# Kernel tuning notes

Hardware: AMD Instinct MI355X
Metric: run time of the kernel (lower is better)

## Reference

```python
import jax, jax.numpy as jnp
import numpy as np

N = 50000   # nodes
E = 600000  # edges
F = 128     # num_node_features
H = 128     # hidden_channels
C = 10      # num_classes
G = 64      # graphs in batch


def setup_inputs() -> dict:
    key = jax.random.key(0)
    ks = jax.random.split(key, 12)
    x = jax.random.normal(ks[0], (N, F), jnp.float32)
    edge_index = jax.random.randint(ks[1], (2, E), 0, N, dtype=jnp.int32)
    batch = jnp.sort(jax.random.randint(ks[2], (N,), 0, G, dtype=jnp.int32))
    def glorot(k, shape):
        lim = np.sqrt(6.0 / (shape[0] + shape[1])).astype(np.float32)
        return jax.random.uniform(k, shape, jnp.float32, -lim, lim)
    return {
        "x": x,
        "edge_index": edge_index,
        "batch": batch,
        "W1": glorot(ks[3], (F, H)), "b1": jnp.zeros((H,), jnp.float32),
        "W2": glorot(ks[4], (H, H)), "b2": jnp.zeros((H,), jnp.float32),
        "W3": glorot(ks[5], (H, H)), "b3": jnp.zeros((H,), jnp.float32),
        "Wl": glorot(ks[6], (H, C)), "bl": jnp.zeros((C,), jnp.float32),
    }


def reference(x, edge_index, batch, W1, b1, W2, b2, W3, b3, Wl, bl):
    # GCNConv: add self-loops, symmetric degree normalization D^-1/2 A D^-1/2
    src0, dst0 = edge_index[0], edge_index[1]
    loop = jnp.arange(N, dtype=src0.dtype)
    src = jnp.concatenate([src0, loop])
    dst = jnp.concatenate([dst0, loop])
    deg = jax.ops.segment_sum(jnp.ones_like(dst, jnp.float32), dst, num_segments=N)
    dinv = jnp.where(deg > 0, jax.lax.rsqrt(deg), 0.0)
    norm = dinv[src] * dinv[dst]  # [E+N]

    def conv(h, W, b):
        h = h @ W                                  # [N, H] transform first (PyG GCNConv)
        msg = h[src] * norm[:, None]               # gather + normalize
        return jax.ops.segment_sum(msg, dst, num_segments=N) + b  # scatter-add

    h = jax.nn.relu(conv(x, W1, b1))
    h = jax.nn.relu(conv(h, W2, b2))
    h = conv(h, W3, b3)

    # global_mean_pool over batch ids
    counts = jax.ops.segment_sum(jnp.ones((N,), jnp.float32), batch, num_segments=G)
    pooled = jax.ops.segment_sum(h, batch, num_segments=G) / jnp.maximum(counts, 1.0)[:, None]
    return pooled @ Wl + bl  # [G, C]
```

## Files before the change

### kernel.cpp

```cpp
#include <hip/hip_runtime.h>
#include <hip/hip_bf16.h>

#define NN 50000
#define EE 600000
#define FF 128
#define HH 128
#define CC 10
#define GG 64
#define SB 256
#define NBSCAN ((NN + SB - 1) / SB)

typedef unsigned int uint32;
typedef unsigned short ushort16;
typedef __attribute__((ext_vector_type(8))) short short8;
typedef __attribute__((ext_vector_type(4))) float f32x4;

__device__ __forceinline__ ushort16 f2bf(float f) {
    __hip_bfloat16 b = __float2bfloat16(f);
    return *reinterpret_cast<ushort16*>(&b);
}
__device__ __forceinline__ uint32 pack2bf(float a, float b) {
    return (uint32)f2bf(a) | ((uint32)f2bf(b) << 16);
}
__device__ __forceinline__ int q8(float f) {
    return __float2int_rn(fminf(fmaxf(f * 16.f, -127.f), 127.f)) & 255;
}

__global__ void count_deg(const int* __restrict__ dst, int* __restrict__ deg) {
    int e = blockIdx.x * blockDim.x + threadIdx.x;
    if (e < EE) atomicAdd(&deg[dst[e]], 1);
}

__global__ __launch_bounds__(SB) void scan_block(const int* __restrict__ deg,
                                                 int* __restrict__ row_ptr,
                                                 int* __restrict__ bsum,
                                                 float* __restrict__ dinv) {
    __shared__ int sm[SB];
    int t = threadIdx.x;
    int i = blockIdx.x * SB + t;
    int v = (i < NN) ? deg[i] : 0;
    if (i < NN) dinv[i] = rsqrtf((float)(v + 1));
    sm[t] = v;
    __syncthreads();
    for (int off = 1; off < SB; off <<= 1) {
        int add = (t >= off) ? sm[t - off] : 0;
        __syncthreads();
        sm[t] += add;
        __syncthreads();
    }
    if (i < NN) row_ptr[i] = sm[t] - v;
    if (t == SB - 1) bsum[blockIdx.x] = sm[t];
}

__global__ void scan_bsum(int* __restrict__ bsum, int nb) {
    __shared__ int sm[256];
    int t = threadIdx.x;
    int v = (t < nb) ? bsum[t] : 0;
    sm[t] = v;
    __syncthreads();
    for (int off = 1; off < 256; off <<= 1) {
        int add = (t >= off) ? sm[t - off] : 0;
        __syncthreads();
        sm[t] += add;
        __syncthreads();
    }
    if (t < nb) bsum[t] = sm[t] - v;
}

__global__ __launch_bounds__(SB) void scan_add_tw(int* __restrict__ row_ptr,
                                                  const int* __restrict__ bsum,
                                                  const float* __restrict__ W1,
                                                  const float* __restrict__ W2,
                                                  const float* __restrict__ W3,
                                                  ushort16* __restrict__ T1,
                                                  ushort16* __restrict__ T2,
                                                  ushort16* __restrict__ T3) {
    int b = blockIdx.x;
    if (b < NBSCAN) {
        int i = b * SB + threadIdx.x;
        if (i < NN) row_ptr[i] += bsum[b];
        if (i == 0) row_ptr[NN] = EE;
    } else {
        int bi = b - NBSCAN;
        int wi = bi >> 4;
        const float* W = (wi == 0) ? W1 : (wi == 1) ? W2 : W3;
        ushort16* T = (wi == 0) ? T1 : (wi == 1) ? T2 : T3;
        int base = (bi & 15) * 256 + threadIdx.x;
#pragma unroll
        for (int i = 0; i < 4; i++) {
            int idx = base + i * 4096;
            int col = idx & 127;
            int k = idx >> 7;
            T[col * 128 + k] = f2bf(W[k * 128 + col]);
        }
    }
}

__global__ void fill_csr(const int* __restrict__ src, const int* __restrict__ dst,
                         const int* __restrict__ row_ptr, int* __restrict__ cursor,
                         const float* __restrict__ dinv,
                         int2* __restrict__ csr_en) {
    int e = blockIdx.x * blockDim.x + threadIdx.x;
    if (e < EE) {
        int s = src[e], d = dst[e];
        int pos = row_ptr[d] + atomicAdd(&cursor[d], 1);
        csr_en[pos] = make_int2(s * 128, __float_as_int(dinv[s] * dinv[d] * 0.0625f));
    }
}

__global__ __launch_bounds__(256) void gemm_x(const float* __restrict__ A,
                                              const ushort16* __restrict__ Wt,
                                              uint32* __restrict__ zout) {
    __shared__ char lds[34816];
    int t = threadIdx.x;
    int w = t >> 6, l = t & 63;
    int lrow = l & 15, g = l >> 4;
    int rowBase = blockIdx.x * 64;
    int arow = rowBase + w * 16 + lrow;
    short8 afr[4];
    const char* Ab = (const char*)A;
    bool inb = arow < NN;
#pragma unroll
    for (int s = 0; s < 4; s++) {
        if (inb) {
            float4 f0 = *(const float4*)(Ab + (size_t)arow * 512 + s * 128 + g * 32);
            float4 f1 = *(const float4*)(Ab + (size_t)arow * 512 + s * 128 + g * 32 + 16);
            union { short8 s8; uint32 u[4]; } cv;
            cv.u[0] = pack2bf(f0.x, f0.y);
            cv.u[1] = pack2bf(f0.z, f0.w);
            cv.u[2] = pack2bf(f1.x, f1.y);
            cv.u[3] = pack2bf(f1.z, f1.w);
            afr[s] = cv.s8;
        } else {
            short8 z = {0, 0, 0, 0, 0, 0, 0, 0};
            afr[s] = z;
        }
    }
    const char* Wb = (const char*)Wt;
#pragma unroll
    for (int i = 0; i < 8; i++) {
        int idx = t + i * 256;
        int col = idx >> 4, c16 = idx & 15;
        *(uint4*)(lds + col * 272 + c16 * 16) = *(const uint4*)(Wb + col * 256 + c16 * 16);
    }
    __syncthreads();
    f32x4 acc[8];
#pragma unroll
    for (int c = 0; c < 8; c++) { f32x4 z = {0.f, 0.f, 0.f, 0.f}; acc[c] = z; }
#pragma unroll
    for (int s = 0; s < 4; s++) {
#pragma unroll
        for (int c = 0; c < 8; c++) {
            short8 b = *(const short8*)(lds + (c * 16 + lrow) * 272 + s * 64 + g * 16);
            acc[c] = __builtin_amdgcn_mfma_f32_16x16x32_bf16(afr[s], b, acc[c], 0, 0, 0);
        }
    }
    __syncthreads();
    char* myl = lds + w * 8448;
#pragma unroll
    for (int c = 0; c < 8; c++) {
#pragma unroll
        for (int j = 0; j < 4; j++) {
            *(float*)(myl + (g * 4 + j) * 528 + (c * 16 + lrow) * 4) = acc[c][j];
        }
    }
    __syncthreads();
#pragma unroll
    for (int j = 0; j < 8; j++) {
        int rl = (l >> 5) + 2 * j;
        int ch = l & 31;
        float4 v = *(const float4*)(myl + rl * 528 + ch * 16);
        int grow = rowBase + w * 16 + rl;
        if (grow < NN) {
            uint32 u = q8(v.x) | (q8(v.y) << 8) | (q8(v.z) << 16) | (q8(v.w) << 24);
            zout[(size_t)grow * 32 + ch] = u;
        }
    }
}

#define AGG_FMA8(c, v)                                              \
    {                                                               \
        float nm = __int_as_float((c).y);                           \
        a0 += nm * (float)((int)((v).x << 24) >> 24);               \
        a1 += nm * (float)((int)((v).x << 16) >> 24);               \
        a2 += nm * (float)((int)((v).x << 8) >> 24);                \
        a3 += nm * (float)((int)(v).x >> 24);                       \
        a4 += nm * (float)((int)((v).y << 24) >> 24);               \
        a5 += nm * (float)((int)((v).y << 16) >> 24);               \
        a6 += nm * (float)((int)((v).y << 8) >> 24);                \
        a7 += nm * (float)((int)(v).y >> 24);                       \
    }

__global__ __launch_bounds__(256) void fused_agg_gemm(const uint32* __restrict__ zin,
                                                      const int* __restrict__ row_ptr,
                                                      const int2* __restrict__ csr_en,
                                                      const float* __restrict__ dinv,
                                                      const float* __restrict__ bias,
                                                      const ushort16* __restrict__ Wt,
                                                      uint32* __restrict__ zout) {
    __shared__ char ldsW[34816];
    __shared__ char ldsA[17408];
    int t = threadIdx.x;
    const char* Wb = (const char*)Wt;
#pragma unroll
    for (int i = 0; i < 8; i++) {
        int idx = t + i * 256;
        int col = idx >> 4, c16 = idx & 15;
        *(uint4*)(ldsW + col * 272 + c16 * 16) = *(const uint4*)(Wb + col * 256 + c16 * 16);
    }
    int grp = t >> 4, ll = t & 15;
    int rowBase = blockIdx.x * 64;
    const char* base = (const char*)zin;
    int boff = ll << 3;
    for (int i = 0; i < 4; i++) {
        int lr = grp * 4 + i;
        int n = rowBase + lr;
        uint4 packed = make_uint4(0, 0, 0, 0);
        if (n < NN) {
            float dn = dinv[n];
            float w2 = dn * dn * 0.0625f;
            float a0, a1, a2, a3, a4, a5, a6, a7;
            {
                uint2 u = *(const uint2*)(base + (size_t)n * 128 + boff);
                a0 = w2 * (float)((int)(u.x << 24) >> 24);
                a1 = w2 * (float)((int)(u.x << 16) >> 24);
                a2 = w2 * (float)((int)(u.x << 8) >> 24);
                a3 = w2 * (float)((int)u.x >> 24);
                a4 = w2 * (float)((int)(u.y << 24) >> 24);
                a5 = w2 * (float)((int)(u.y << 16) >> 24);
                a6 = w2 * (float)((int)(u.y << 8) >> 24);
                a7 = w2 * (float)((int)u.y >> 24);
            }
            int s = row_ptr[n], e = row_ptr[n + 1];
            int k = s;
            if (k + 4 <= e) {
                int2 c0 = csr_en[k], c1 = csr_en[k + 1], c2 = csr_en[k + 2], c3 = csr_en[k + 3];
                uint2 v0 = *(const uint2*)(base + (size_t)(uint32)c0.x + boff);
                uint2 v1 = *(const uint2*)(base + (size_t)(uint32)c1.x + boff);
                uint2 v2 = *(const uint2*)(base + (size_t)(uint32)c2.x + boff);
                uint2 v3 = *(const uint2*)(base + (size_t)(uint32)c3.x + boff);
                k += 4;
                for (; k + 4 <= e; k += 4) {
                    int2 d0 = csr_en[k], d1 = csr_en[k + 1], d2 = csr_en[k + 2], d3 = csr_en[k + 3];
                    uint2 w0 = *(const uint2*)(base + (size_t)(uint32)d0.x + boff);
                    uint2 w1 = *(const uint2*)(base + (size_t)(uint32)d1.x + boff);
                    uint2 w2_ = *(const uint2*)(base + (size_t)(uint32)d2.x + boff);
                    uint2 w3 = *(const uint2*)(base + (size_t)(uint32)d3.x + boff);
                    AGG_FMA8(c0, v0); AGG_FMA8(c1, v1); AGG_FMA8(c2, v2); AGG_FMA8(c3, v3);
                    c0 = d0; c1 = d1; c2 = d2; c3 = d3;
                    v0 = w0; v1 = w1; v2 = w2_; v3 = w3;
                }
                AGG_FMA8(c0, v0); AGG_FMA8(c1, v1); AGG_FMA8(c2, v2); AGG_FMA8(c3, v3);
            }
            for (; k < e; k++) {
                int2 c0 = csr_en[k];
                uint2 v0 = *(const uint2*)(base + (size_t)(uint32)c0.x + boff);
                AGG_FMA8(c0, v0);
            }
            float4 bA = *(const float4*)(bias + ll * 8);
            float4 bB = *(const float4*)(bias + ll * 8 + 4);
            a0 = fmaxf(a0 + bA.x, 0.f); a1 = fmaxf(a1 + bA.y, 0.f);
            a2 = fmaxf(a2 + bA.z, 0.f); a3 = fmaxf(a3 + bA.w, 0.f);
            a4 = fmaxf(a4 + bB.x, 0.f); a5 = fmaxf(a5 + bB.y, 0.f);
            a6 = fmaxf(a6 + bB.z, 0.f); a7 = fmaxf(a7 + bB.w, 0.f);
            packed.x = pack2bf(a0, a1); packed.y = pack2bf(a2, a3);
            packed.z = pack2bf(a4, a5); packed.w = pack2bf(a6, a7);
        }
        *(uint4*)(ldsA + lr * 272 + ll * 16) = packed;
    }
    __syncthreads();
    int w = t >> 6, l = t & 63;
    int lrow = l & 15, g = l >> 4;
    short8 afr[4];
#pragma unroll
    for (int s = 0; s < 4; s++) {
        afr[s] = *(const short8*)(ldsA + (w * 16 + lrow) * 272 + s * 64 + g * 16);
    }
    f32x4 acc[8];
#pragma unroll
    for (int c = 0; c < 8; c++) { f32x4 z = {0.f, 0.f, 0.f, 0.f}; acc[c] = z; }
#pragma unroll
    for (int s = 0; s < 4; s++) {
#pragma unroll
        for (int c = 0; c < 8; c++) {
            short8 b = *(const short8*)(ldsW + (c * 16 + lrow) * 272 + s * 64 + g * 16);
            acc[c] = __builtin_amdgcn_mfma_f32_16x16x32_bf16(afr[s], b, acc[c], 0, 0, 0);
        }
    }
    __syncthreads();
    char* myl = ldsW + w * 8448;
#pragma unroll
    for (int c = 0; c < 8; c++) {
#pragma unroll
        for (int j = 0; j < 4; j++) {
            *(float*)(myl + (g * 4 + j) * 528 + (c * 16 + lrow) * 4) = acc[c][j];
        }
    }
    __syncthreads();
#pragma unroll
    for (int j = 0; j < 8; j++) {
        int rl = (l >> 5) + 2 * j;
        int ch = l & 31;
        float4 v = *(const float4*)(myl + rl * 528 + ch * 16);
        int grow = rowBase + w * 16 + rl;
        if (grow < NN) {
            uint32 u = q8(v.x) | (q8(v.y) << 8) | (q8(v.z) << 16) | (q8(v.w) << 24);
            zout[(size_t)grow * 32 + ch] = u;
        }
    }
}

#define AGG_FMA4(c, v)                                             \
    {                                                              \
        float nm = __int_as_float((c).y);                          \
        a0 += nm * (float)((int)((v) << 24) >> 24);                \
        a1 += nm * (float)((int)((v) << 16) >> 24);                \
        a2 += nm * (float)((int)((v) << 8) >> 24);                 \
        a3 += nm * (float)((int)(v) >> 24);                        \
    }

__global__ __launch_bounds__(256) void aggregate_pool(const uint32* __restrict__ z8,
                                                      const int* __restrict__ row_ptr,
                                                      const int2* __restrict__ csr_en,
                                                      const float* __restrict__ dinv,
                                                      const float* __restrict__ bias,
                                                      float* __restrict__ pooled,
                                                      const int* __restrict__ batch) {
    int grp = threadIdx.x >> 5;
    int ll  = threadIdx.x & 31;
    int n = blockIdx.x * 8 + grp;
    const char* base = (const char*)z8;
    int boff = ll << 2;
    float dn = dinv[n];
    float w2 = dn * dn * 0.0625f;
    float a0, a1, a2, a3;
    {
        uint32 u = *(const uint32*)(base + (size_t)n * 128 + boff);
        a0 = w2 * (float)((int)(u << 24) >> 24);
        a1 = w2 * (float)((int)(u << 16) >> 24);
        a2 = w2 * (float)((int)(u << 8) >> 24);
        a3 = w2 * (float)((int)u >> 24);
    }
    int s = row_ptr[n], e = row_ptr[n + 1];
    int k = s;
    if (k + 4 <= e) {
        int2 c0 = csr_en[k], c1 = csr_en[k + 1], c2 = csr_en[k + 2], c3 = csr_en[k + 3];
        uint32 v0 = *(const uint32*)(base + (size_t)(uint32)c0.x + boff);
        uint32 v1 = *(const uint32*)(base + (size_t)(uint32)c1.x + boff);
        uint32 v2 = *(const uint32*)(base + (size_t)(uint32)c2.x + boff);
        uint32 v3 = *(const uint32*)(base + (size_t)(uint32)c3.x + boff);
        k += 4;
        for (; k + 4 <= e; k += 4) {
            int2 d0 = csr_en[k], d1 = csr_en[k + 1], d2 = csr_en[k + 2], d3 = csr_en[k + 3];
            uint32 w0 = *(const uint32*)(base + (size_t)(uint32)d0.x + boff);
            uint32 w1 = *(const uint32*)(base + (size_t)(uint32)d1.x + boff);
            uint32 w2_ = *(const uint32*)(base + (size_t)(uint32)d2.x + boff);
            uint32 w3 = *(const uint32*)(base + (size_t)(uint32)d3.x + boff);
            AGG_FMA4(c0, v0); AGG_FMA4(c1, v1); AGG_FMA4(c2, v2); AGG_FMA4(c3, v3);
            c0 = d0; c1 = d1; c2 = d2; c3 = d3;
            v0 = w0; v1 = w1; v2 = w2_; v3 = w3;
        }
        AGG_FMA4(c0, v0); AGG_FMA4(c1, v1); AGG_FMA4(c2, v2); AGG_FMA4(c3, v3);
    }
    for (; k < e; k++) {
        int2 c0 = csr_en[k];
        uint32 v0 = *(const uint32*)(base + (size_t)(uint32)c0.x + boff);
        AGG_FMA4(c0, v0);
    }
    float4 b4 = *(const float4*)(bias + (ll << 2));
    a0 += b4.x; a1 += b4.y; a2 += b4.z; a3 += b4.w;
    __shared__ float psum[2][128];
    __shared__ int sgmin;
    int g = batch[n];
    if (threadIdx.x == 0) sgmin = g;
    psum[threadIdx.x >> 7][threadIdx.x & 127] = 0.f;
    __syncthreads();
    int slot = g - sgmin;
    if (slot < 2) {
        float* p = &psum[slot][ll << 2];
        atomicAdd(p + 0, a0); atomicAdd(p + 1, a1);
        atomicAdd(p + 2, a2); atomicAdd(p + 3, a3);
    } else {
        float* p = &pooled[g * HH + (ll << 2)];
        atomicAdd(p + 0, a0); atomicAdd(p + 1, a1);
        atomicAdd(p + 2, a2); atomicAdd(p + 3, a3);
    }
    __syncthreads();
    int sl = threadIdx.x >> 7, f = threadIdx.x & 127;
    float v = psum[sl][f];
    int gg = sgmin + sl;
    if (v != 0.f && gg < GG) atomicAdd(&pooled[gg * HH + f], v);
}

__global__ __launch_bounds__(128) void final_linear(const float* __restrict__ pooled,
                                                    const int* __restrict__ batch,
                                                    const float* __restrict__ Wl,
                                                    const float* __restrict__ bl,
                                                    float* __restrict__ out) {
    int g = blockIdx.x;
    int t = threadIdx.x;
    __shared__ float pm[128];
    __shared__ int cnt_s;
    if (t == 0) {
        int lo = 0, hi = NN;
        while (lo < hi) { int m = (lo + hi) >> 1; if (batch[m] < g) lo = m + 1; else hi = m; }
        int s = lo;
        lo = 0; hi = NN;
        while (lo < hi) { int m = (lo + hi) >> 1; if (batch[m] < g + 1) lo = m + 1; else hi = m; }
        int c = lo - s;
        cnt_s = c > 0 ? c : 1;
    }
    __syncthreads();
    pm[t] = pooled[g * HH + t] / (float)cnt_s;
    __syncthreads();
    if (t < CC) {
        float o = bl[t];
        for (int f = 0; f < 128; f++) o += pm[f] * Wl[f * CC + t];
        out[g * CC + t] = o;
    }
}

extern "C" void kernel_launch(void* const* d_in, const int* in_sizes, int n_in,
                              void* d_out, int out_size, void* d_ws, size_t ws_size,
                              hipStream_t stream) {
    const float* x    = (const float*)d_in[0];
    const int*   ei   = (const int*)d_in[1];
    const int*   bat  = (const int*)d_in[2];
    const float* W1   = (const float*)d_in[3];
    const float* b1   = (const float*)d_in[4];
    const float* W2   = (const float*)d_in[5];
    const float* b2   = (const float*)d_in[6];
    const float* W3   = (const float*)d_in[7];
    const float* b3   = (const float*)d_in[8];
    const float* Wl   = (const float*)d_in[9];
    const float* bl   = (const float*)d_in[10];
    float* out = (float*)d_out;

    const int* src = ei;
    const int* dst = ei + EE;

    char* ws = (char*)d_ws;
    size_t off = 0;
    auto take = [&](size_t bytes) -> char* {
        char* p = ws + off;
        off += (bytes + 255) & ~(size_t)255;
        return p;
    };
    int*      deg     = (int*)take((size_t)NN * 4);
    int*      cursor  = (int*)take((size_t)NN * 4);
    float*    pooled  = (float*)take((size_t)GG * HH * 4);
    float*    dinv    = (float*)take((size_t)NN * 4);
    int*      row_ptr = (int*)take((size_t)(NN + 1) * 4);
    int*      bsum    = (int*)take((size_t)256 * 4);
    int2*     csr_en  = (int2*)take((size_t)EE * 8);
    ushort16* Wt1     = (ushort16*)take((size_t)HH * HH * 2);
    ushort16* Wt2     = (ushort16*)take((size_t)HH * HH * 2);
    ushort16* Wt3     = (ushort16*)take((size_t)HH * HH * 2);
    uint32*   zA      = (uint32*)take((size_t)NN * HH);
    uint32*   zB      = (uint32*)take((size_t)NN * HH);

    const size_t clr = ((size_t)NN * 4 + 255 & ~(size_t)255) * 2 +
                       ((size_t)GG * HH * 4);
    hipMemsetAsync(deg, 0, clr, stream);

    count_deg<<<(EE + 255) / 256, 256, 0, stream>>>(dst, deg);
    scan_block<<<NBSCAN, SB, 0, stream>>>(deg, row_ptr, bsum, dinv);
    scan_bsum<<<1, 256, 0, stream>>>(bsum, NBSCAN);
    scan_add_tw<<<NBSCAN + 48, SB, 0, stream>>>(row_ptr, bsum, W1, W2, W3, Wt1, Wt2, Wt3);
    fill_csr<<<(EE + 255) / 256, 256, 0, stream>>>(src, dst, row_ptr, cursor, dinv, csr_en);

    const int gemmBlocks = (NN + 63) / 64;
    gemm_x<<<gemmBlocks, 256, 0, stream>>>(x, Wt1, zA);
    fused_agg_gemm<<<gemmBlocks, 256, 0, stream>>>(zA, row_ptr, csr_en, dinv, b1, Wt2, zB);
    fused_agg_gemm<<<gemmBlocks, 256, 0, stream>>>(zB, row_ptr, csr_en, dinv, b2, Wt3, zA);
    aggregate_pool<<<NN / 8, 256, 0, stream>>>(zA, row_ptr, csr_en, dinv, b3, pooled, bat);

    final_linear<<<GG, 128, 0, stream>>>(pooled, bat, Wl, bl, out);
}
```

Measured before the change: 226.8 us.

## Split fused aggregate+GEMM into separate aggregate and MFMA GEMM kernels

Replaces the fused per-64-row aggregate-then-GEMM kernel with a 32-lane-per-node aggregate kernel that writes bf16 activations to a global buffer, followed by a standalone MFMA GEMM kernel. The per-edge norm drops the dinv[d] factor, which is applied once per node, and fill_csr uses a cursor preinitialised to row_ptr so it needs one fewer load. The goal is higher gather parallelism and occupancy in aggregation, without the heavy LDS use and serialization of the fused kernel. In exchange, each layer adds a bf16 round trip through global memory and an extra kernel launch.

```diff
diff --git a/kernel.cpp b/kernel.cpp
--- a/kernel.cpp
+++ b/kernel.cpp
@@ -68,6 +68,7 @@
 }
 
 __global__ __launch_bounds__(SB) void scan_add_tw(int* __restrict__ row_ptr,
+                                                  int* __restrict__ cursor,
                                                   const int* __restrict__ bsum,
                                                   const float* __restrict__ W1,
                                                   const float* __restrict__ W2,
@@ -78,7 +79,11 @@
     int b = blockIdx.x;
     if (b < NBSCAN) {
         int i = b * SB + threadIdx.x;
-        if (i < NN) row_ptr[i] += bsum[b];
+        if (i < NN) {
+            int v = row_ptr[i] + bsum[b];
+            row_ptr[i] = v;
+            cursor[i] = v;
+        }
         if (i == 0) row_ptr[NN] = EE;
     } else {
         int bi = b - NBSCAN;
@@ -97,14 +102,14 @@
 }
 
 __global__ void fill_csr(const int* __restrict__ src, const int* __restrict__ dst,
-                         const int* __restrict__ row_ptr, int* __restrict__ cursor,
+                         int* __restrict__ cursor,
                          const float* __restrict__ dinv,
                          int2* __restrict__ csr_en) {
     int e = blockIdx.x * blockDim.x + threadIdx.x;
     if (e < EE) {
         int s = src[e], d = dst[e];
-        int pos = row_ptr[d] + atomicAdd(&cursor[d], 1);
-        csr_en[pos] = make_int2(s * 128, __float_as_int(dinv[s] * dinv[d] * 0.0625f));
+        int pos = atomicAdd(&cursor[d], 1);
+        csr_en[pos] = make_int2(s * 128, __float_as_int(dinv[s] * 0.0625f));
     }
 }
 
@@ -178,117 +183,48 @@
     }
 }
 
-#define AGG_FMA8(c, v)                                              \
-    {                                                               \
-        float nm = __int_as_float((c).y);                           \
-        a0 += nm * (float)((int)((v).x << 24) >> 24);               \
-        a1 += nm * (float)((int)((v).x << 16) >> 24);               \
-        a2 += nm * (float)((int)((v).x << 8) >> 24);                \
-        a3 += nm * (float)((int)(v).x >> 24);                       \
-        a4 += nm * (float)((int)((v).y << 24) >> 24);               \
-        a5 += nm * (float)((int)((v).y << 16) >> 24);               \
-        a6 += nm * (float)((int)((v).y << 8) >> 24);                \
-        a7 += nm * (float)((int)(v).y >> 24);                       \
-    }
-
-__global__ __launch_bounds__(256) void fused_agg_gemm(const uint32* __restrict__ zin,
-                                                      const int* __restrict__ row_ptr,
-                                                      const int2* __restrict__ csr_en,
-                                                      const float* __restrict__ dinv,
-                                                      const float* __restrict__ bias,
-                                                      const ushort16* __restrict__ Wt,
-                                                      uint32* __restrict__ zout) {
-    __shared__ char ldsW[34816];
-    __shared__ char ldsA[17408];
+__global__ __launch_bounds__(256) void gemm_h(const ushort16* __restrict__ A,
+                                              const ushort16* __restrict__ Wt,
+                                              uint32* __restrict__ zout) {
+    __shared__ char lds[34816];
     int t = threadIdx.x;
+    int w = t >> 6, l = t & 63;
+    int lrow = l & 15, g = l >> 4;
+    int rowBase = blockIdx.x * 64;
+    int arow = rowBase + w * 16 + lrow;
+    short8 afr[4];
+    const char* Ab = (const char*)A;
+    bool inb = arow < NN;
+#pragma unroll
+    for (int s = 0; s < 4; s++) {
+        if (inb) {
+            afr[s] = *(const short8*)(Ab + (size_t)arow * 256 + s * 64 + g * 16);
+        } else {
+            short8 z = {0, 0, 0, 0, 0, 0, 0, 0};
+            afr[s] = z;
+        }
+    }
     const char* Wb = (const char*)Wt;
 #pragma unroll
     for (int i = 0; i < 8; i++) {
         int idx = t + i * 256;
         int col = idx >> 4, c16 = idx & 15;
-        *(uint4*)(ldsW + col * 272 + c16 * 16) = *(const uint4*)(Wb + col * 256 + c16 * 16);
-    }
-    int grp = t >> 4, ll = t & 15;
-    int rowBase = blockIdx.x * 64;
-    const char* base = (const char*)zin;
-    int boff = ll << 3;
-    for (int i = 0; i < 4; i++) {
-        int lr = grp * 4 + i;
-        int n = rowBase + lr;
-        uint4 packed = make_uint4(0, 0, 0, 0);
-        if (n < NN) {
-            float dn = dinv[n];
-            float w2 = dn * dn * 0.0625f;
-            float a0, a1, a2, a3, a4, a5, a6, a7;
-            {
-                uint2 u = *(const uint2*)(base + (size_t)n * 128 + boff);
-                a0 = w2 * (float)((int)(u.x << 24) >> 24);
-                a1 = w2 * (float)((int)(u.x << 16) >> 24);
-                a2 = w2 * (float)((int)(u.x << 8) >> 24);
-                a3 = w2 * (float)((int)u.x >> 24);
-                a4 = w2 * (float)((int)(u.y << 24) >> 24);
-                a5 = w2 * (float)((int)(u.y << 16) >> 24);
-                a6 = w2 * (float)((int)(u.y << 8) >> 24);
-                a7 = w2 * (float)((int)u.y >> 24);
-            }
-            int s = row_ptr[n], e = row_ptr[n + 1];
-            int k = s;
-            if (k + 4 <= e) {
-                int2 c0 = csr_en[k], c1 = csr_en[k + 1], c2 = csr_en[k + 2], c3 = csr_en[k + 3];
-                uint2 v0 = *(const uint2*)(base + (size_t)(uint32)c0.x + boff);
-                uint2 v1 = *(const uint2*)(base + (size_t)(uint32)c1.x + boff);
-                uint2 v2 = *(const uint2*)(base + (size_t)(uint32)c2.x + boff);
-                uint2 v3 = *(const uint2*)(base + (size_t)(uint32)c3.x + boff);
-                k += 4;
-                for (; k + 4 <= e; k += 4) {
-                    int2 d0 = csr_en[k], d1 = csr_en[k + 1], d2 = csr_en[k + 2], d3 = csr_en[k + 3];
-                    uint2 w0 = *(const uint2*)(base + (size_t)(uint32)d0.x + boff);
-                    uint2 w1 = *(const uint2*)(base + (size_t)(uint32)d1.x + boff);
-                    uint2 w2_ = *(const uint2*)(base + (size_t)(uint32)d2.x + boff);
-                    uint2 w3 = *(const uint2*)(base + (size_t)(uint32)d3.x + boff);
-                    AGG_FMA8(c0, v0); AGG_FMA8(c1, v1); AGG_FMA8(c2, v2); AGG_FMA8(c3, v3);
-                    c0 = d0; c1 = d1; c2 = d2; c3 = d3;
-                    v0 = w0; v1 = w1; v2 = w2_; v3 = w3;
-                }
-                AGG_FMA8(c0, v0); AGG_FMA8(c1, v1); AGG_FMA8(c2, v2); AGG_FMA8(c3, v3);
-            }
-            for (; k < e; k++) {
-                int2 c0 = csr_en[k];
-                uint2 v0 = *(const uint2*)(base + (size_t)(uint32)c0.x + boff);
-                AGG_FMA8(c0, v0);
-            }
-            float4 bA = *(const float4*)(bias + ll * 8);
-            float4 bB = *(const float4*)(bias + ll * 8 + 4);
-            a0 = fmaxf(a0 + bA.x, 0.f); a1 = fmaxf(a1 + bA.y, 0.f);
-            a2 = fmaxf(a2 + bA.z, 0.f); a3 = fmaxf(a3 + bA.w, 0.f);
-            a4 = fmaxf(a4 + bB.x, 0.f); a5 = fmaxf(a5 + bB.y, 0.f);
-            a6 = fmaxf(a6 + bB.z, 0.f); a7 = fmaxf(a7 + bB.w, 0.f);
-            packed.x = pack2bf(a0, a1); packed.y = pack2bf(a2, a3);
-            packed.z = pack2bf(a4, a5); packed.w = pack2bf(a6, a7);
-        }
-        *(uint4*)(ldsA + lr * 272 + ll * 16) = packed;
-    }
-    __syncthreads();
-    int w = t >> 6, l = t & 63;
-    int lrow = l & 15, g = l >> 4;
-    short8 afr[4];
+        *(uint4*)(lds + col * 272 + c16 * 16) = *(const uint4*)(Wb + col * 256 + c16 * 16);
+    }
+    __syncthreads();
+    f32x4 acc[8];
+#pragma unroll
+    for (int c = 0; c < 8; c++) { f32x4 z = {0.f, 0.f, 0.f, 0.f}; acc[c] = z; }
 #pragma unroll
     for (int s = 0; s < 4; s++) {
-        afr[s] = *(const short8*)(ldsA + (w * 16 + lrow) * 272 + s * 64 + g * 16);
-    }
-    f32x4 acc[8];
-#pragma unroll
-    for (int c = 0; c < 8; c++) { f32x4 z = {0.f, 0.f, 0.f, 0.f}; acc[c] = z; }
-#pragma unroll
-    for (int s = 0; s < 4; s++) {
 #pragma unroll
         for (int c = 0; c < 8; c++) {
-            short8 b = *(const short8*)(ldsW + (c * 16 + lrow) * 272 + s * 64 + g * 16);
+            short8 b = *(const short8*)(lds + (c * 16 + lrow) * 272 + s * 64 + g * 16);
             acc[c] = __builtin_amdgcn_mfma_f32_16x16x32_bf16(afr[s], b, acc[c], 0, 0, 0);
         }
     }
     __syncthreads();
-    char* myl = ldsW + w * 8448;
+    char* myl = lds + w * 8448;
 #pragma unroll
     for (int c = 0; c < 8; c++) {
 #pragma unroll
@@ -319,28 +255,23 @@
         a3 += nm * (float)((int)(v) >> 24);                        \
     }
 
-__global__ __launch_bounds__(256) void aggregate_pool(const uint32* __restrict__ z8,
-                                                      const int* __restrict__ row_ptr,
-                                                      const int2* __restrict__ csr_en,
-                                                      const float* __restrict__ dinv,
-                                                      const float* __restrict__ bias,
-                                                      float* __restrict__ pooled,
-                                                      const int* __restrict__ batch) {
+template <int MODE>
+__global__ __launch_bounds__(256) void aggregate(const uint32* __restrict__ z8,
+                                                 const int* __restrict__ row_ptr,
+                                                 const int2* __restrict__ csr_en,
+                                                 const float* __restrict__ dinv,
+                                                 const float* __restrict__ bias,
+                                                 ushort16* __restrict__ out,
+                                                 float* __restrict__ pooled,
+                                                 const int* __restrict__ batch) {
     int grp = threadIdx.x >> 5;
     int ll  = threadIdx.x & 31;
     int n = blockIdx.x * 8 + grp;
     const char* base = (const char*)z8;
     int boff = ll << 2;
+    uint32 uself = *(const uint32*)(base + (size_t)n * 128 + boff);
     float dn = dinv[n];
-    float w2 = dn * dn * 0.0625f;
-    float a0, a1, a2, a3;
-    {
-        uint32 u = *(const uint32*)(base + (size_t)n * 128 + boff);
-        a0 = w2 * (float)((int)(u << 24) >> 24);
-        a1 = w2 * (float)((int)(u << 16) >> 24);
-        a2 = w2 * (float)((int)(u << 8) >> 24);
-        a3 = w2 * (float)((int)u >> 24);
-    }
+    float a0 = 0.f, a1 = 0.f, a2 = 0.f, a3 = 0.f;
     int s = row_ptr[n], e = row_ptr[n + 1];
     int k = s;
     if (k + 4 <= e) {
@@ -367,29 +298,40 @@
         uint32 v0 = *(const uint32*)(base + (size_t)(uint32)c0.x + boff);
         AGG_FMA4(c0, v0);
     }
+    float ws = dn * dn * 0.0625f;
     float4 b4 = *(const float4*)(bias + (ll << 2));
-    a0 += b4.x; a1 += b4.y; a2 += b4.z; a3 += b4.w;
-    __shared__ float psum[2][128];
-    __shared__ int sgmin;
-    int g = batch[n];
-    if (threadIdx.x == 0) sgmin = g;
-    psum[threadIdx.x >> 7][threadIdx.x & 127] = 0.f;
-    __syncthreads();
-    int slot = g - sgmin;
-    if (slot < 2) {
-        float* p = &psum[slot][ll << 2];
-        atomicAdd(p + 0, a0); atomicAdd(p + 1, a1);
-        atomicAdd(p + 2, a2); atomicAdd(p + 3, a3);
-    } else {
-        float* p = &pooled[g * HH + (ll << 2)];
-        atomicAdd(p + 0, a0); atomicAdd(p + 1, a1);
-        atomicAdd(p + 2, a2); atomicAdd(p + 3, a3);
-    }
-    __syncthreads();
-    int sl = threadIdx.x >> 7, f = threadIdx.x & 127;
-    float v = psum[sl][f];
-    int gg = sgmin + sl;
-    if (v != 0.f && gg < GG) atomicAdd(&pooled[gg * HH + f], v);
+    a0 = dn * a0 + ws * (float)((int)(uself << 24) >> 24) + b4.x;
+    a1 = dn * a1 + ws * (float)((int)(uself << 16) >> 24) + b4.y;
+    a2 = dn * a2 + ws * (float)((int)(uself << 8) >> 24) + b4.z;
+    a3 = dn * a3 + ws * (float)((int)uself >> 24) + b4.w;
+    if (MODE == 0) {
+        a0 = fmaxf(a0, 0.f); a1 = fmaxf(a1, 0.f); a2 = fmaxf(a2, 0.f); a3 = fmaxf(a3, 0.f);
+        uint2 o = make_uint2(pack2bf(a0, a1), pack2bf(a2, a3));
+        *(uint2*)((char*)out + (size_t)n * 256 + (ll << 3)) = o;
+    }
+    if (MODE == 2) {
+        __shared__ float psum[2][128];
+        __shared__ int sgmin;
+        int g = batch[n];
+        if (threadIdx.x == 0) sgmin = g;
+        psum[threadIdx.x >> 7][threadIdx.x & 127] = 0.f;
+        __syncthreads();
+        int slot = g - sgmin;
+        if (slot < 2) {
+            float* p = &psum[slot][ll << 2];
+            atomicAdd(p + 0, a0); atomicAdd(p + 1, a1);
+            atomicAdd(p + 2, a2); atomicAdd(p + 3, a3);
+        } else {
+            float* p = &pooled[g * HH + (ll << 2)];
+            atomicAdd(p + 0, a0); atomicAdd(p + 1, a1);
+            atomicAdd(p + 2, a2); atomicAdd(p + 3, a3);
+        }
+        __syncthreads();
+        int sl = threadIdx.x >> 7, f = threadIdx.x & 127;
+        float v = psum[sl][f];
+        int gg = sgmin + sl;
+        if (v != 0.f && gg < GG) atomicAdd(&pooled[gg * HH + f], v);
+    }
 }
 
 __global__ __launch_bounds__(128) void final_linear(const float* __restrict__ pooled,
@@ -447,8 +389,8 @@
         return p;
     };
     int*      deg     = (int*)take((size_t)NN * 4);
+    float*    pooled  = (float*)take((size_t)GG * HH * 4);
     int*      cursor  = (int*)take((size_t)NN * 4);
-    float*    pooled  = (float*)take((size_t)GG * HH * 4);
     float*    dinv    = (float*)take((size_t)NN * 4);
     int*      row_ptr = (int*)take((size_t)(NN + 1) * 4);
     int*      bsum    = (int*)take((size_t)256 * 4);
@@ -458,22 +400,25 @@
     ushort16* Wt3     = (ushort16*)take((size_t)HH * HH * 2);
     uint32*   zA      = (uint32*)take((size_t)NN * HH);
     uint32*   zB      = (uint32*)take((size_t)NN * HH);
-
-    const size_t clr = ((size_t)NN * 4 + 255 & ~(size_t)255) * 2 +
-                       ((size_t)GG * HH * 4);
+    ushort16* bufH    = (ushort16*)take((size_t)NN * HH * 2);
+
+    const size_t clr = (((size_t)NN * 4 + 255) & ~(size_t)255) + (size_t)GG * HH * 4;
     hipMemsetAsync(deg, 0, clr, stream);
 
     count_deg<<<(EE + 255) / 256, 256, 0, stream>>>(dst, deg);
     scan_block<<<NBSCAN, SB, 0, stream>>>(deg, row_ptr, bsum, dinv);
     scan_bsum<<<1, 256, 0, stream>>>(bsum, NBSCAN);
-    scan_add_tw<<<NBSCAN + 48, SB, 0, stream>>>(row_ptr, bsum, W1, W2, W3, Wt1, Wt2, Wt3);
-    fill_csr<<<(EE + 255) / 256, 256, 0, stream>>>(src, dst, row_ptr, cursor, dinv, csr_en);
+    scan_add_tw<<<NBSCAN + 48, SB, 0, stream>>>(row_ptr, cursor, bsum, W1, W2, W3, Wt1, Wt2, Wt3);
+    fill_csr<<<(EE + 255) / 256, 256, 0, stream>>>(src, dst, cursor, dinv, csr_en);
 
     const int gemmBlocks = (NN + 63) / 64;
+    const int aggBlocks  = NN / 8;
     gemm_x<<<gemmBlocks, 256, 0, stream>>>(x, Wt1, zA);
-    fused_agg_gemm<<<gemmBlocks, 256, 0, stream>>>(zA, row_ptr, csr_en, dinv, b1, Wt2, zB);
-    fused_agg_gemm<<<gemmBlocks, 256, 0, stream>>>(zB, row_ptr, csr_en, dinv, b2, Wt3, zA);
-    aggregate_pool<<<NN / 8, 256, 0, stream>>>(zA, row_ptr, csr_en, dinv, b3, pooled, bat);
+    aggregate<0><<<aggBlocks, 256, 0, stream>>>(zA, row_ptr, csr_en, dinv, b1, bufH, pooled, bat);
+    gemm_h<<<gemmBlocks, 256, 0, stream>>>(bufH, Wt2, zB);
+    aggregate<0><<<aggBlocks, 256, 0, stream>>>(zB, row_ptr, csr_en, dinv, b2, bufH, pooled, bat);
+    gemm_h<<<gemmBlocks, 256, 0, stream>>>(bufH, Wt3, zA);
+    aggregate<2><<<aggBlocks, 256, 0, stream>>>(zA, row_ptr, csr_en, dinv, b3, bufH, pooled, bat);
 
     final_linear<<<GG, 128, 0, stream>>>(pooled, bat, Wl, bl, out);
 }
```

Result: faster. 197.7 us (-12.8%).
